# Performance work log

Hardware: AMD Instinct MI355X
Metric: run time of the kernel (lower is better)

The kernel has to match this reference:

```python
import jax, jax.numpy as jnp
import numpy as np

H, KV, D, HID = 32, 8, 128, 4096
B, S = 1, 2048
ROPE_THETA = 10000.0


def setup_inputs() -> dict:
    key = jax.random.key(0)
    ks = jax.random.split(key, 5)
    std = 0.02
    return {
        "x": jax.random.normal(ks[0], (B, S, HID), jnp.float32),
        "Wq": jax.random.normal(ks[1], (H * D, HID), jnp.float32) * std,
        "Wk": jax.random.normal(ks[2], (KV * D, HID), jnp.float32) * std,
        "Wv": jax.random.normal(ks[3], (KV * D, HID), jnp.float32) * std,
        "Wo": jax.random.normal(ks[4], (HID, H * D), jnp.float32) * std,
    }


def _rope_cos_sin(seq_len, dim, dtype):
    inv_freq = 1.0 / (ROPE_THETA ** (jnp.arange(0, dim, 2, dtype=jnp.float32) / dim))
    t = jnp.arange(seq_len, dtype=jnp.float32)
    freqs = jnp.einsum("s,d->sd", t, inv_freq)          # [S, D/2]
    emb = jnp.concatenate([freqs, freqs], axis=-1)        # [S, D]
    return jnp.cos(emb).astype(dtype), jnp.sin(emb).astype(dtype)


def _rotate_half(x):
    x1, x2 = jnp.split(x, 2, axis=-1)
    return jnp.concatenate([-x2, x1], axis=-1)


def reference(x, Wq, Wk, Wv, Wo):
    Bx, Sx, _ = x.shape
    q = (x @ Wq.T).reshape(Bx, Sx, H, D).transpose(0, 2, 1, 3)    # [B,H,S,D]
    k = (x @ Wk.T).reshape(Bx, Sx, KV, D).transpose(0, 2, 1, 3)   # [B,KV,S,D]
    v = (x @ Wv.T).reshape(Bx, Sx, KV, D).transpose(0, 2, 1, 3)

    cos, sin = _rope_cos_sin(Sx, D, x.dtype)                       # [S,D]
    q = q * cos + _rotate_half(q) * sin
    k = k * cos + _rotate_half(k) * sin

    rep = H // KV
    k = jnp.repeat(k, rep, axis=1)                                 # [B,H,S,D]
    v = jnp.repeat(v, rep, axis=1)

    scale = 1.0 / jnp.sqrt(jnp.asarray(D, x.dtype))
    scores = jnp.einsum("bhqd,bhkd->bhqk", q, k) * scale           # [B,H,S,S]
    causal = jnp.tril(jnp.ones((Sx, Sx), dtype=bool))
    scores = jnp.where(causal, scores, jnp.asarray(-1e30, x.dtype))
    attn = jax.nn.softmax(scores, axis=-1)
    out = jnp.einsum("bhqk,bhkd->bhqd", attn, v)                   # [B,H,S,D]
    out = out.transpose(0, 2, 1, 3).reshape(Bx, Sx, H * D)
    return out @ Wo.T
```

## Files before the change

kernel.cpp:

```cpp
#include <hip/hip_runtime.h>

typedef unsigned short u16;
typedef unsigned int u32;

using f32x4  = __attribute__((ext_vector_type(4))) float;
using f32x16 = __attribute__((ext_vector_type(16))) float;
using bf16x8 = __attribute__((ext_vector_type(8))) __bf16;

#define S_LEN 2048
#define HID_DIM 4096
#define NH 32
#define NKV 8
#define HD 128
#define QKVN 6144

__device__ __forceinline__ u16 f2b(float f) {
  union { float f; u32 u; } v; v.f = f;
  u32 r = (v.u + 0x7FFFu + ((v.u >> 16) & 1u)) >> 16;
  return (u16)r;
}
__device__ __forceinline__ float b2f(u16 b) {
  union { u32 u; float f; } v; v.u = ((u32)b) << 16;
  return v.f;
}

__device__ __forceinline__ u32 cvtpk_bf16(float lo, float hi) {
  u32 r;
  asm("v_cvt_pk_bf16_f32 %0, %1, %2" : "=v"(r) : "v"(lo), "v"(hi));
  return r;
}
__device__ __forceinline__ void plane_swap(u32& a, u32& b) {
  asm volatile("v_permlane32_swap_b32 %0, %1" : "+v"(a), "+v"(b));
}

#define AS1 __attribute__((address_space(1)))
#define AS3 __attribute__((address_space(3)))
__device__ __forceinline__ void gl_lds16(const u16* g, u16* l) {
  __builtin_amdgcn_global_load_lds((const AS1 u32*)g, (AS3 u32*)l, 16, 0, 0);
}

#define SBAR  __builtin_amdgcn_s_barrier()
#define SCHED0 __builtin_amdgcn_sched_barrier(0)
#define LGKM0 do { asm volatile("s_waitcnt lgkmcnt(0)" ::: "memory"); SCHED0; } while (0)
#define PRIO1 __builtin_amdgcn_s_setprio(1)
#define PRIO0 __builtin_amdgcn_s_setprio(0)

template <int N> __device__ __forceinline__ void waitv() {
  if constexpr (N == 0) asm volatile("s_waitcnt vmcnt(0)" ::: "memory");
  else if constexpr (N == 6) asm volatile("s_waitcnt vmcnt(6)" ::: "memory");
  else if constexpr (N == 7) asm volatile("s_waitcnt vmcnt(7)" ::: "memory");
  else asm volatile("s_waitcnt vmcnt(0)" ::: "memory");
  SCHED0;
}

__global__ void cast_kernel(const float* __restrict__ src, u16* __restrict__ dst, int n4) {
  int i = blockIdx.x * blockDim.x + threadIdx.x;
  int stride = gridDim.x * blockDim.x;
  for (; i < n4; i += stride) {
    float4 v = ((const float4*)src)[i];
    uint2 o;
    o.x = (u32)f2b(v.x) | ((u32)f2b(v.y) << 16);
    o.y = (u32)f2b(v.z) | ((u32)f2b(v.w) << 16);
    ((uint2*)dst)[i] = o;
  }
}

#define STAGE(DST, SRC, CH, LDK)                                   \
  _Pragma("unroll") for (int c = 0; c < (CH); ++c) {               \
    int d_ = c * 8192 + tid * 16;                                  \
    int rw_ = d_ >> 7;                                             \
    int cb_ = (d_ & 127) ^ ((rw_ & 7) << 4);                       \
    gl_lds16((SRC) + (size_t)rw_ * (LDK) + (cb_ >> 1), (DST) + (d_ >> 1)); \
  }

#define READ_A(ABUF, MLO)                                                     \
  _Pragma("unroll") for (int mm = 0; mm < 4; ++mm)                            \
  _Pragma("unroll") for (int ks = 0; ks < 2; ++ks)                            \
    af[(MLO) + mm][ks] = *(const bf16x8*)((const char*)(ABUF) +               \
      (wmo + ((MLO) + mm) * 16 + lr) * 128 + ((((ks << 2) | lg) ^ lr7) << 4));

#define READ_B(BBUF, KS)                                                      \
  _Pragma("unroll") for (int nn = 0; nn < NF; ++nn)                           \
    bfr[nn][KS] = *(const bf16x8*)((const char*)(BBUF) +                      \
      (wno + nn * 16 + lr) * 128 + (((((KS) << 2) | lg) ^ lr7) << 4));

#define MFMA_Q(MLO, KS)                                                       \
  _Pragma("unroll") for (int mm = 0; mm < 4; ++mm)                            \
  _Pragma("unroll") for (int nn = 0; nn < NF; ++nn)                           \
    acc[(MLO) + mm][nn] = __builtin_amdgcn_mfma_f32_16x16x32_bf16(            \
        af[(MLO) + mm][KS], bfr[nn][KS], acc[(MLO) + mm][nn], 0, 0, 0);

template <int BN, int WN, int CBF>
__global__ __launch_bounds__(512, 2) void gemm8p(
    const u16* __restrict__ A, const u16* __restrict__ B, void* __restrict__ Cout,
    int M, int N, int K)
{
  constexpr int BM = 256;
  constexpr int NF = WN / 16;
  constexpr int LA = BM / 64;
  constexpr int LB = BN / 64;
  constexpr int LT = LA + LB;
  extern __shared__ __align__(16) u16 smem[];
  u16* const As0 = smem;
  u16* const Bs0 = smem + 2 * BM * 64;

  const int tid  = threadIdx.x;
  const int lane = tid & 63;
  const int wave = tid >> 6;
  const int lr  = lane & 15;
  const int lg  = lane >> 4;
  const int lr7 = lane & 7;

  const int nbx = N / BN;
  const int bid = blockIdx.x;
  const int cpx = gridDim.x >> 3;
  const int swz = (bid & 7) * cpx + (bid >> 3);
  const int bm = (swz / nbx) * BM;
  const int bn = (swz % nbx) * BN;
  const int wmo = (wave >> 2) * 128;
  const int wno = (wave & 3) * WN;

  const int NT = K >> 6;

  f32x4 acc[8][NF] = {};
  bf16x8 af[8][2], bfr[NF][2];

  const u16* aP = A + (size_t)bm * K;
  const u16* bP = B + (size_t)bn * K;

  STAGE(As0,               aP,      LA, K);
  STAGE(Bs0,               bP,      LB, K);
  STAGE(As0 + BM * 64,     aP + 64, LA, K);
  STAGE(Bs0 + BN * 64,     bP + 64, LB, K);
  waitv<LT>();
  SBAR; SCHED0;

  for (int t = 0; t < NT; ++t) {
    const int buf = t & 1;
    const u16* ab = As0 + buf * (BM * 64);
    const u16* bb = Bs0 + buf * (BN * 64);
    const bool st = (t + 2 < NT);

    READ_A(ab, 0);
    READ_B(bb, 0);
    SCHED0; SBAR; LGKM0;
    PRIO1; MFMA_Q(0, 0); PRIO0;
    SBAR; SCHED0;

    READ_A(ab, 4);
    READ_B(bb, 1);
    SCHED0; SBAR; LGKM0;
    PRIO1; MFMA_Q(4, 0); PRIO0;
    SBAR; SCHED0;

    if (st) {
      const u16* aS = aP + (size_t)(t + 2) * 64;
      u16* aD = As0 + buf * (BM * 64);
      STAGE(aD, aS, LA, K);
    }
    SCHED0; SBAR;
    PRIO1; MFMA_Q(0, 1); PRIO0;
    SBAR; SCHED0;

    if (st) {
      const u16* bS = bP + (size_t)(t + 2) * 64;
      u16* bD = Bs0 + buf * (BN * 64);
      STAGE(bD, bS, LB, K);
    }
    SCHED0; SBAR;
    PRIO1; MFMA_Q(4, 1); PRIO0;
    if (t + 1 < NT) {
      if (t < NT - 3) waitv<LT>(); else waitv<0>();
    }
    SBAR; SCHED0;
  }

#pragma unroll
  for (int m = 0; m < 8; ++m)
#pragma unroll
    for (int j = 0; j < 4; ++j) {
      int row = bm + wmo + m * 16 + lg * 4 + j;
      size_t base = (size_t)row * N + bn + wno + lr;
      if constexpr (CBF) {
        u16* C = (u16*)Cout;
#pragma unroll
        for (int nn = 0; nn < NF; ++nn) C[base + nn * 16] = f2b(acc[m][nn][j]);
      } else {
        float* C = (float*)Cout;
#pragma unroll
        for (int nn = 0; nn < NF; ++nn) C[base + nn * 16] = acc[m][nn][j];
      }
    }
}

__global__ void rope_qk(const u16* __restrict__ qkv, u16* __restrict__ dst,
                        int col_off, float scale, int frag) {
  int idx = blockIdx.x * blockDim.x + threadIdx.x;
  int i = idx & 63;
  int s = (idx >> 6) & (S_LEN - 1);
  int h = idx >> 17;
  const u16* row = qkv + (size_t)s * QKVN + col_off + h * HD;
  float a = b2f(row[i]);
  float b = b2f(row[i + 64]);
  float invf = __expf(-(float)i * 0.14391156831212787f);
  float f = (float)s * invf;
  float sn, cs;
  sincosf(f, &sn, &cs);
  float o1 = (a * cs - b * sn) * scale;
  float o2 = (b * cs + a * sn) * scale;
  if (frag) {
    int qt = h * 64 + (s >> 5);
    int qq = s & 31;
    int i2 = i + 64;
    dst[((qt * 8 + (i  >> 4)) * 2 + ((i  >> 3) & 1)) * 256 + qq * 8 + (i  & 7)] = f2b(o1);
    dst[((qt * 8 + (i2 >> 4)) * 2 + ((i2 >> 3) & 1)) * 256 + qq * 8 + (i2 & 7)] = f2b(o2);
  } else {
    u16* orow = dst + ((size_t)h * S_LEN + s) * HD;
    orow[i]      = f2b(o1);
    orow[i + 64] = f2b(o2);
  }
}

__global__ __launch_bounds__(256) void vf_pack(const u16* __restrict__ qkv,
                                               u16* __restrict__ VF) {
  __shared__ u16 vlds[32][136];
  const int bid = blockIdx.x;
  const int kv = bid >> 6, t = bid & 63;
  const int tid = threadIdx.x;
  const int r = tid >> 3, d0 = (tid & 7) * 16;
  const u16* src = qkv + (size_t)(t * 32 + r) * QKVN + 5120 + kv * HD + d0;
  *(bf16x8*)&vlds[r][d0]     = *(const bf16x8*)src;
  *(bf16x8*)&vlds[r][d0 + 8] = *(const bf16x8*)(src + 8);
  __syncthreads();
  u16* outt = VF + (size_t)bid * 4096;
#pragma unroll
  for (int g = 0; g < 2; ++g) {
    int G = tid + g * 256;
    int q = G & 31, dt = (G >> 5) & 3, hi2 = (G >> 7) & 1, kc = G >> 8;
    union { u16 u[8]; uint4 v; } o;
#pragma unroll
    for (int e = 0; e < 8; ++e)
      o.u[e] = vlds[kc * 16 + hi2 * 8 + e][dt * 32 + q];
    *(uint4*)&outt[G * 8] = o.v;
  }
}

__global__ __launch_bounds__(256, 2) void attn_fwd(
    const u16* __restrict__ QF,
    const u16* __restrict__ KF,
    const u16* __restrict__ VF,
    u16* __restrict__ Out)
{
  const int tid  = threadIdx.x;
  const int lane = tid & 63;
  const int wv   = tid >> 6;
  const int q31  = lane & 31;
  const int hi   = lane >> 5;
  const int bid  = blockIdx.x;
  const int kvh  = bid & 7;
  const int qi   = 63 - (bid >> 3);
  const int q0   = qi * 32;
  const int h    = kvh * 4 + wv;
  const int nt   = qi + 1;

  const u16* kbase = KF + (size_t)kvh * 64 * 4096 + hi * 256  + q31 * 8;
  const u16* vbase = VF + (size_t)kvh * 64 * 4096 + hi * 1024 + q31 * 8;

  bf16x8 qf[8];
  const u16* qfp = QF + (size_t)(h * 64 + qi) * 4096 + hi * 256 + q31 * 8;
#pragma unroll
  for (int dc = 0; dc < 8; ++dc)
    qf[dc] = *(const bf16x8*)(qfp + dc * 512);

  f32x16 o0 = {}, o1 = {}, o2 = {}, o3 = {};
  float m = -1e30f, lsum = 0.f;

  for (int t = 0; t < nt; ++t) {
    SBAR;

    bf16x8 kf[8];
    const u16* kfp = kbase + (size_t)t * 4096;
#pragma unroll
    for (int dc = 0; dc < 8; ++dc)
      kf[dc] = *(const bf16x8*)(kfp + dc * 512);

    bf16x8 vf[8];
    const u16* vfp = vbase + (size_t)t * 4096;
#pragma unroll
    for (int i = 0; i < 8; ++i)
      vf[i] = *(const bf16x8*)(vfp + (i & 1) * 2048 + (i >> 1) * 256);

    f32x16 st = {};
    PRIO1;
#pragma unroll
    for (int dc = 0; dc < 8; ++dc)
      st = __builtin_amdgcn_mfma_f32_32x32x16_bf16(kf[dc], qf[dc], st, 0, 0, 0);
    PRIO0;

    if (t == nt - 1) {
#pragma unroll
      for (int r = 0; r < 16; ++r) {
        int kk = (r & 3) + 8 * (r >> 2) + 4 * hi;
        if (kk > q31) st[r] = -1e30f;
      }
    }

    float a0 = fmaxf(st[0], st[1]),   a1 = fmaxf(st[2], st[3]);
    float a2 = fmaxf(st[4], st[5]),   a3 = fmaxf(st[6], st[7]);
    float a4 = fmaxf(st[8], st[9]),   a5 = fmaxf(st[10], st[11]);
    float a6 = fmaxf(st[12], st[13]), a7 = fmaxf(st[14], st[15]);
    a0 = fmaxf(a0, a1); a2 = fmaxf(a2, a3); a4 = fmaxf(a4, a5); a6 = fmaxf(a6, a7);
    float pmax = fmaxf(fmaxf(a0, a2), fmaxf(a4, a6));
    pmax = fmaxf(pmax, __shfl_xor(pmax, 32));

    if (__any(pmax > m + 8.f)) {
      float mn = fmaxf(m, pmax);
      float sf = exp2f(m - mn);
      m = mn;
      lsum *= sf;
#pragma unroll
      for (int r = 0; r < 16; ++r) { o0[r] *= sf; o1[r] *= sf; o2[r] *= sf; o3[r] *= sf; }
    }

    float ev[16];
#pragma unroll
    for (int r = 0; r < 16; ++r) ev[r] = exp2f(st[r] - m);
    float s0 = (ev[0] + ev[1]) + (ev[2] + ev[3]);
    float s1 = (ev[4] + ev[5]) + (ev[6] + ev[7]);
    float s2 = (ev[8] + ev[9]) + (ev[10] + ev[11]);
    float s3 = (ev[12] + ev[13]) + (ev[14] + ev[15]);
    float ps = (s0 + s1) + (s2 + s3);
    ps += __shfl_xor(ps, 32);
    lsum += ps;

    u32 c0 = cvtpk_bf16(ev[0],  ev[1]),  c1 = cvtpk_bf16(ev[2],  ev[3]);
    u32 c2 = cvtpk_bf16(ev[4],  ev[5]),  c3 = cvtpk_bf16(ev[6],  ev[7]);
    u32 c4 = cvtpk_bf16(ev[8],  ev[9]),  c5 = cvtpk_bf16(ev[10], ev[11]);
    u32 c6 = cvtpk_bf16(ev[12], ev[13]), c7 = cvtpk_bf16(ev[14], ev[15]);
    plane_swap(c0, c2);
    plane_swap(c1, c3);
    plane_swap(c4, c6);
    plane_swap(c5, c7);
    union { u32 u[4]; bf16x8 v; } pb0u, pb1u;
    pb0u.u[0] = c0; pb0u.u[1] = c1; pb0u.u[2] = c2; pb0u.u[3] = c3;
    pb1u.u[0] = c4; pb1u.u[1] = c5; pb1u.u[2] = c6; pb1u.u[3] = c7;

    PRIO1;
    o0 = __builtin_amdgcn_mfma_f32_32x32x16_bf16(vf[0], pb0u.v, o0, 0, 0, 0);
    o1 = __builtin_amdgcn_mfma_f32_32x32x16_bf16(vf[2], pb0u.v, o1, 0, 0, 0);
    o2 = __builtin_amdgcn_mfma_f32_32x32x16_bf16(vf[4], pb0u.v, o2, 0, 0, 0);
    o3 = __builtin_amdgcn_mfma_f32_32x32x16_bf16(vf[6], pb0u.v, o3, 0, 0, 0);
    o0 = __builtin_amdgcn_mfma_f32_32x32x16_bf16(vf[1], pb1u.v, o0, 0, 0, 0);
    o1 = __builtin_amdgcn_mfma_f32_32x32x16_bf16(vf[3], pb1u.v, o1, 0, 0, 0);
    o2 = __builtin_amdgcn_mfma_f32_32x32x16_bf16(vf[5], pb1u.v, o2, 0, 0, 0);
    o3 = __builtin_amdgcn_mfma_f32_32x32x16_bf16(vf[7], pb1u.v, o3, 0, 0, 0);
    PRIO0;
  }

  float inv = 1.0f / lsum;
  u16* orow = Out + (size_t)(q0 + q31) * (NH * HD) + h * HD;
#pragma unroll
  for (int dt = 0; dt < 4; ++dt) {
    const f32x16& oo = dt == 0 ? o0 : dt == 1 ? o1 : dt == 2 ? o2 : o3;
#pragma unroll
    for (int g = 0; g < 4; ++g) {
      ushort4 pk;
      pk.x = f2b(oo[g * 4 + 0] * inv);
      pk.y = f2b(oo[g * 4 + 1] * inv);
      pk.z = f2b(oo[g * 4 + 2] * inv);
      pk.w = f2b(oo[g * 4 + 3] * inv);
      *(ushort4*)&orow[dt * 32 + 8 * g + 4 * hi] = pk;
    }
  }
}

extern "C" void kernel_launch(void* const* d_in, const int* in_sizes, int n_in,
                              void* d_out, int out_size, void* d_ws, size_t ws_size,
                              hipStream_t stream) {
  const float* x  = (const float*)d_in[0];
  const float* Wq = (const float*)d_in[1];
  const float* Wk = (const float*)d_in[2];
  const float* Wv = (const float*)d_in[3];
  const float* Wo = (const float*)d_in[4];
  float* out = (float*)d_out;

  char* ws = (char*)d_ws;
  u16* xb   = (u16*)(ws);
  u16* wqkv = (u16*)(ws + (16ull << 20));
  u16* wo_b = (u16*)(ws + (64ull << 20));
  u16* qkvb = (u16*)(ws + (96ull << 20));
  u16* qb   = (u16*)(ws + (16ull << 20));
  u16* kfb  = (u16*)(ws + (32ull << 20));
  u16* vfb  = (u16*)(ws + (36ull << 20));
  u16* ao   = (u16*)(ws);

  const int smem_q = (256 + 192) * 256;
  const int smem_o = (256 + 128) * 256;
  hipFuncSetAttribute((const void*)&gemm8p<192, 48, 1>,
                      hipFuncAttributeMaxDynamicSharedMemorySize, smem_q);
  hipFuncSetAttribute((const void*)&gemm8p<128, 32, 0>,
                      hipFuncAttributeMaxDynamicSharedMemorySize, smem_o);

  cast_kernel<<<4096, 256, 0, stream>>>(x,  xb,   (2048 * 4096) / 4);
  cast_kernel<<<4096, 256, 0, stream>>>(Wq, wqkv, (4096 * 4096) / 4);
  cast_kernel<<<2048, 256, 0, stream>>>(Wk, wqkv + (size_t)4096 * 4096, (1024 * 4096) / 4);
  cast_kernel<<<2048, 256, 0, stream>>>(Wv, wqkv + (size_t)5120 * 4096, (1024 * 4096) / 4);
  cast_kernel<<<4096, 256, 0, stream>>>(Wo, wo_b, (4096 * 4096) / 4);

  gemm8p<192, 48, 1><<<256, 512, smem_q, stream>>>(xb, wqkv, qkvb, 2048, 6144, 4096);

  rope_qk<<<(32 * 2048 * 64) / 256, 256, 0, stream>>>(qkvb, qb,  0,    0.12751741f, 1);
  rope_qk<<<(8  * 2048 * 64) / 256, 256, 0, stream>>>(qkvb, kfb, 4096, 1.0f,        1);
  vf_pack<<<512, 256, 0, stream>>>(qkvb, vfb);

  attn_fwd<<<512, 256, 0, stream>>>(qb, kfb, vfb, ao);

  gemm8p<128, 32, 0><<<256, 512, smem_o, stream>>>(ao, wo_b, out, 2048, 4096, 4096);
}
```

Baseline: 328.1 us.

## Replace 8-wave 256-row GEMM with 4-wave 128-row tile GEMM

Both projection GEMMs switch from a 512-thread, 256-row block tile to a 256-thread, 128-row block tile with 2x2 waves, which doubles the grid to 512 blocks. The inner loop is simplified: two K-substeps, each reading A and B fragments and issuing all MFMAs, followed by staging the next K tile and waiting. The aim is better CU occupancy and load balance with more blocks and fewer registers per thread. The cost is lower operand reuse per block, more global and LDS traffic per FLOP, and less interleaving of global loads with MFMA work.

```diff
diff --git a/kernel.cpp b/kernel.cpp
--- a/kernel.cpp
+++ b/kernel.cpp
@@ -46,10 +46,12 @@
 #define PRIO0 __builtin_amdgcn_s_setprio(0)
 
 template <int N> __device__ __forceinline__ void waitv() {
-  if constexpr (N == 0) asm volatile("s_waitcnt vmcnt(0)" ::: "memory");
-  else if constexpr (N == 6) asm volatile("s_waitcnt vmcnt(6)" ::: "memory");
-  else if constexpr (N == 7) asm volatile("s_waitcnt vmcnt(7)" ::: "memory");
-  else asm volatile("s_waitcnt vmcnt(0)" ::: "memory");
+  if constexpr (N == 0)       asm volatile("s_waitcnt vmcnt(0)"  ::: "memory");
+  else if constexpr (N == 6)  asm volatile("s_waitcnt vmcnt(6)"  ::: "memory");
+  else if constexpr (N == 7)  asm volatile("s_waitcnt vmcnt(7)"  ::: "memory");
+  else if constexpr (N == 8)  asm volatile("s_waitcnt vmcnt(8)"  ::: "memory");
+  else if constexpr (N == 10) asm volatile("s_waitcnt vmcnt(10)" ::: "memory");
+  else                        asm volatile("s_waitcnt vmcnt(0)"  ::: "memory");
   SCHED0;
 }
 
@@ -65,44 +67,47 @@
   }
 }
 
-#define STAGE(DST, SRC, CH, LDK)                                   \
+
+#define STG(DST, SRC, CH, LDK)                                     \
   _Pragma("unroll") for (int c = 0; c < (CH); ++c) {               \
-    int d_ = c * 8192 + tid * 16;                                  \
+    int d_ = c * 4096 + tid * 16;                                  \
     int rw_ = d_ >> 7;                                             \
     int cb_ = (d_ & 127) ^ ((rw_ & 7) << 4);                       \
     gl_lds16((SRC) + (size_t)rw_ * (LDK) + (cb_ >> 1), (DST) + (d_ >> 1)); \
   }
 
-#define READ_A(ABUF, MLO)                                                     \
+#define RD_A(ABUF, KS)                                                        \
   _Pragma("unroll") for (int mm = 0; mm < 4; ++mm)                            \
-  _Pragma("unroll") for (int ks = 0; ks < 2; ++ks)                            \
-    af[(MLO) + mm][ks] = *(const bf16x8*)((const char*)(ABUF) +               \
-      (wmo + ((MLO) + mm) * 16 + lr) * 128 + ((((ks << 2) | lg) ^ lr7) << 4));
-
-#define READ_B(BBUF, KS)                                                      \
+    af[mm] = *(const bf16x8*)((const char*)(ABUF) +                           \
+      (wmo + mm * 16 + lr) * 128 + ((((KS) * 4 + lg) ^ lr7) << 4));
+
+#define RD_B(BBUF, KS)                                                        \
   _Pragma("unroll") for (int nn = 0; nn < NF; ++nn)                           \
-    bfr[nn][KS] = *(const bf16x8*)((const char*)(BBUF) +                      \
-      (wno + nn * 16 + lr) * 128 + (((((KS) << 2) | lg) ^ lr7) << 4));
-
-#define MFMA_Q(MLO, KS)                                                       \
+    bfr[nn] = *(const bf16x8*)((const char*)(BBUF) +                          \
+      (wno + nn * 16 + lr) * 128 + ((((KS) * 4 + lg) ^ lr7) << 4));
+
+#define MFMA_ALL                                                              \
   _Pragma("unroll") for (int mm = 0; mm < 4; ++mm)                            \
   _Pragma("unroll") for (int nn = 0; nn < NF; ++nn)                           \
-    acc[(MLO) + mm][nn] = __builtin_amdgcn_mfma_f32_16x16x32_bf16(            \
-        af[(MLO) + mm][KS], bfr[nn][KS], acc[(MLO) + mm][nn], 0, 0, 0);
-
-template <int BN, int WN, int CBF>
-__global__ __launch_bounds__(512, 2) void gemm8p(
+    acc[mm][nn] = __builtin_amdgcn_mfma_f32_16x16x32_bf16(                    \
+        af[mm], bfr[nn], acc[mm][nn], 0, 0, 0);
+
+template <int BN, int CBF>
+__global__ __launch_bounds__(256, 2) void gemm2b(
     const u16* __restrict__ A, const u16* __restrict__ B, void* __restrict__ Cout,
     int M, int N, int K)
 {
-  constexpr int BM = 256;
+  constexpr int BM = 128;
+  constexpr int WN = BN / 2;
   constexpr int NF = WN / 16;
-  constexpr int LA = BM / 64;
-  constexpr int LB = BN / 64;
+  constexpr int LA = (BM * 128) / 4096;
+  constexpr int LB = (BN * 128) / 4096;
   constexpr int LT = LA + LB;
+  constexpr int ASZ = BM * 64;
+  constexpr int BSZ = BN * 64;
   extern __shared__ __align__(16) u16 smem[];
   u16* const As0 = smem;
-  u16* const Bs0 = smem + 2 * BM * 64;
+  u16* const Bs0 = smem + 2 * ASZ;
 
   const int tid  = threadIdx.x;
   const int lane = tid & 63;
@@ -117,78 +122,64 @@
   const int swz = (bid & 7) * cpx + (bid >> 3);
   const int bm = (swz / nbx) * BM;
   const int bn = (swz % nbx) * BN;
-  const int wmo = (wave >> 2) * 128;
-  const int wno = (wave & 3) * WN;
+  const int wmo = (wave >> 1) * 64;
+  const int wno = (wave & 1) * WN;
 
   const int NT = K >> 6;
 
-  f32x4 acc[8][NF] = {};
-  bf16x8 af[8][2], bfr[NF][2];
+  f32x4 acc[4][NF] = {};
+  bf16x8 af[4], bfr[NF];
 
   const u16* aP = A + (size_t)bm * K;
   const u16* bP = B + (size_t)bn * K;
 
-  STAGE(As0,               aP,      LA, K);
-  STAGE(Bs0,               bP,      LB, K);
-  STAGE(As0 + BM * 64,     aP + 64, LA, K);
-  STAGE(Bs0 + BN * 64,     bP + 64, LB, K);
+  STG(As0,        aP,      LA, K);
+  STG(Bs0,        bP,      LB, K);
+  STG(As0 + ASZ,  aP + 64, LA, K);
+  STG(Bs0 + BSZ,  bP + 64, LB, K);
   waitv<LT>();
   SBAR; SCHED0;
 
   for (int t = 0; t < NT; ++t) {
     const int buf = t & 1;
-    const u16* ab = As0 + buf * (BM * 64);
-    const u16* bb = Bs0 + buf * (BN * 64);
+    const u16* ab = As0 + buf * ASZ;
+    const u16* bb = Bs0 + buf * BSZ;
+
+    RD_A(ab, 0); RD_B(bb, 0);
+    SCHED0; SBAR; LGKM0;
+    PRIO1; MFMA_ALL; PRIO0;
+    SBAR; SCHED0;
+
+    RD_A(ab, 1); RD_B(bb, 1);
+    SCHED0; SBAR; LGKM0;
+    PRIO1; MFMA_ALL; PRIO0;
+    SBAR; SCHED0;
+
     const bool st = (t + 2 < NT);
-
-    READ_A(ab, 0);
-    READ_B(bb, 0);
-    SCHED0; SBAR; LGKM0;
-    PRIO1; MFMA_Q(0, 0); PRIO0;
+    if (st) {
+      STG(As0 + buf * ASZ, aP + (size_t)(t + 2) * 64, LA, K);
+      STG(Bs0 + buf * BSZ, bP + (size_t)(t + 2) * 64, LB, K);
+    }
+    if (t + 1 < NT) {
+      if (st) waitv<LT>(); else waitv<0>();
+    }
     SBAR; SCHED0;
-
-    READ_A(ab, 4);
-    READ_B(bb, 1);
-    SCHED0; SBAR; LGKM0;
-    PRIO1; MFMA_Q(4, 0); PRIO0;
-    SBAR; SCHED0;
-
-    if (st) {
-      const u16* aS = aP + (size_t)(t + 2) * 64;
-      u16* aD = As0 + buf * (BM * 64);
-      STAGE(aD, aS, LA, K);
-    }
-    SCHED0; SBAR;
-    PRIO1; MFMA_Q(0, 1); PRIO0;
-    SBAR; SCHED0;
-
-    if (st) {
-      const u16* bS = bP + (size_t)(t + 2) * 64;
-      u16* bD = Bs0 + buf * (BN * 64);
-      STAGE(bD, bS, LB, K);
-    }
-    SCHED0; SBAR;
-    PRIO1; MFMA_Q(4, 1); PRIO0;
-    if (t + 1 < NT) {
-      if (t < NT - 3) waitv<LT>(); else waitv<0>();
-    }
-    SBAR; SCHED0;
-  }
-
-#pragma unroll
-  for (int m = 0; m < 8; ++m)
+  }
+
+#pragma unroll
+  for (int mm = 0; mm < 4; ++mm)
 #pragma unroll
     for (int j = 0; j < 4; ++j) {
-      int row = bm + wmo + m * 16 + lg * 4 + j;
+      int row = bm + wmo + mm * 16 + lg * 4 + j;
       size_t base = (size_t)row * N + bn + wno + lr;
       if constexpr (CBF) {
         u16* C = (u16*)Cout;
 #pragma unroll
-        for (int nn = 0; nn < NF; ++nn) C[base + nn * 16] = f2b(acc[m][nn][j]);
+        for (int nn = 0; nn < NF; ++nn) C[base + nn * 16] = f2b(acc[mm][nn][j]);
       } else {
         float* C = (float*)Cout;
 #pragma unroll
-        for (int nn = 0; nn < NF; ++nn) C[base + nn * 16] = acc[m][nn][j];
+        for (int nn = 0; nn < NF; ++nn) C[base + nn * 16] = acc[mm][nn][j];
       }
     }
 }
@@ -394,11 +385,11 @@
   u16* vfb  = (u16*)(ws + (36ull << 20));
   u16* ao   = (u16*)(ws);
 
-  const int smem_q = (256 + 192) * 256;
-  const int smem_o = (256 + 128) * 256;
-  hipFuncSetAttribute((const void*)&gemm8p<192, 48, 1>,
+  const int smem_q = (128 + 192) * 64 * 2 * 2;
+  const int smem_o = (128 + 128) * 64 * 2 * 2;
+  hipFuncSetAttribute((const void*)&gemm2b<192, 1>,
                       hipFuncAttributeMaxDynamicSharedMemorySize, smem_q);
-  hipFuncSetAttribute((const void*)&gemm8p<128, 32, 0>,
+  hipFuncSetAttribute((const void*)&gemm2b<128, 0>,
                       hipFuncAttributeMaxDynamicSharedMemorySize, smem_o);
 
   cast_kernel<<<4096, 256, 0, stream>>>(x,  xb,   (2048 * 4096) / 4);
@@ -407,7 +398,7 @@
   cast_kernel<<<2048, 256, 0, stream>>>(Wv, wqkv + (size_t)5120 * 4096, (1024 * 4096) / 4);
   cast_kernel<<<4096, 256, 0, stream>>>(Wo, wo_b, (4096 * 4096) / 4);
 
-  gemm8p<192, 48, 1><<<256, 512, smem_q, stream>>>(xb, wqkv, qkvb, 2048, 6144, 4096);
+  gemm2b<192, 1><<<512, 256, smem_q, stream>>>(xb, wqkv, qkvb, 2048, 6144, 4096);
 
   rope_qk<<<(32 * 2048 * 64) / 256, 256, 0, stream>>>(qkvb, qb,  0,    0.12751741f, 1);
   rope_qk<<<(8  * 2048 * 64) / 256, 256, 0, stream>>>(qkvb, kfb, 4096, 1.0f,        1);
@@ -415,5 +406,5 @@
 
   attn_fwd<<<512, 256, 0, stream>>>(qb, kfb, vfb, ao);
 
-  gemm8p<128, 32, 0><<<256, 512, smem_o, stream>>>(ao, wo_b, out, 2048, 4096, 4096);
-}
+  gemm2b<128, 0><<<512, 256, smem_o, stream>>>(ao, wo_b, out, 2048, 4096, 4096);
+}
```

Measured after the change: 343.5 us. +4.7%, slower.

## Restructure GEMM main loop to cut barriers and batch LDS reads per k-slice

Applied to the files above, without the earlier changes.

Reorders the double-buffered GEMM inner loop so all A and B fragments for one k-slice are read from LDS at once, followed by all MFMAs for that slice. Both next-tile global-to-LDS stages are issued together after a single barrier, replacing the earlier four-phase schedule that had a barrier around every MFMA group. The aim is less barrier stall time and less interleaving overhead, at the cost of coarser overlap between LDS reads, global loads and MFMA. It also keeps more fragment registers live at once.

```diff
diff --git a/kernel.cpp b/kernel.cpp
--- a/kernel.cpp
+++ b/kernel.cpp
@@ -46,10 +46,10 @@
 #define PRIO0 __builtin_amdgcn_s_setprio(0)
 
 template <int N> __device__ __forceinline__ void waitv() {
-  if constexpr (N == 0) asm volatile("s_waitcnt vmcnt(0)" ::: "memory");
+  if constexpr (N == 0)      asm volatile("s_waitcnt vmcnt(0)" ::: "memory");
   else if constexpr (N == 6) asm volatile("s_waitcnt vmcnt(6)" ::: "memory");
   else if constexpr (N == 7) asm volatile("s_waitcnt vmcnt(7)" ::: "memory");
-  else asm volatile("s_waitcnt vmcnt(0)" ::: "memory");
+  else                       asm volatile("s_waitcnt vmcnt(0)" ::: "memory");
   SCHED0;
 }
 
@@ -65,6 +65,7 @@
   }
 }
 
+
 #define STAGE(DST, SRC, CH, LDK)                                   \
   _Pragma("unroll") for (int c = 0; c < (CH); ++c) {               \
     int d_ = c * 8192 + tid * 16;                                  \
@@ -73,13 +74,12 @@
     gl_lds16((SRC) + (size_t)rw_ * (LDK) + (cb_ >> 1), (DST) + (d_ >> 1)); \
   }
 
-#define READ_A(ABUF, MLO)                                                     \
+#define RDA(ABUF, MLO, KS)                                                    \
   _Pragma("unroll") for (int mm = 0; mm < 4; ++mm)                            \
-  _Pragma("unroll") for (int ks = 0; ks < 2; ++ks)                            \
-    af[(MLO) + mm][ks] = *(const bf16x8*)((const char*)(ABUF) +               \
-      (wmo + ((MLO) + mm) * 16 + lr) * 128 + ((((ks << 2) | lg) ^ lr7) << 4));
-
-#define READ_B(BBUF, KS)                                                      \
+    af[(MLO) + mm][KS] = *(const bf16x8*)((const char*)(ABUF) +               \
+      (wmo + ((MLO) + mm) * 16 + lr) * 128 + (((((KS) << 2) | lg) ^ lr7) << 4));
+
+#define RDB(BBUF, KS)                                                         \
   _Pragma("unroll") for (int nn = 0; nn < NF; ++nn)                           \
     bfr[nn][KS] = *(const bf16x8*)((const char*)(BBUF) +                      \
       (wno + nn * 16 + lr) * 128 + (((((KS) << 2) | lg) ^ lr7) << 4));
@@ -128,10 +128,10 @@
   const u16* aP = A + (size_t)bm * K;
   const u16* bP = B + (size_t)bn * K;
 
-  STAGE(As0,               aP,      LA, K);
-  STAGE(Bs0,               bP,      LB, K);
-  STAGE(As0 + BM * 64,     aP + 64, LA, K);
-  STAGE(Bs0 + BN * 64,     bP + 64, LB, K);
+  STAGE(As0,           aP,      LA, K);
+  STAGE(Bs0,           bP,      LB, K);
+  STAGE(As0 + BM * 64, aP + 64, LA, K);
+  STAGE(Bs0 + BN * 64, bP + 64, LB, K);
   waitv<LT>();
   SBAR; SCHED0;
 
@@ -141,36 +141,20 @@
     const u16* bb = Bs0 + buf * (BN * 64);
     const bool st = (t + 2 < NT);
 
-    READ_A(ab, 0);
-    READ_B(bb, 0);
-    SCHED0; SBAR; LGKM0;
-    PRIO1; MFMA_Q(0, 0); PRIO0;
-    SBAR; SCHED0;
-
-    READ_A(ab, 4);
-    READ_B(bb, 1);
-    SCHED0; SBAR; LGKM0;
-    PRIO1; MFMA_Q(4, 0); PRIO0;
-    SBAR; SCHED0;
+    RDA(ab, 0, 0); RDA(ab, 4, 0); RDB(bb, 0);
+    LGKM0;
+    PRIO1; MFMA_Q(0, 0); MFMA_Q(4, 0); PRIO0;
+    RDA(ab, 0, 1); RDA(ab, 4, 1); RDB(bb, 1);
+    LGKM0;
+    SBAR;
 
     if (st) {
-      const u16* aS = aP + (size_t)(t + 2) * 64;
-      u16* aD = As0 + buf * (BM * 64);
-      STAGE(aD, aS, LA, K);
-    }
-    SCHED0; SBAR;
-    PRIO1; MFMA_Q(0, 1); PRIO0;
-    SBAR; SCHED0;
-
-    if (st) {
-      const u16* bS = bP + (size_t)(t + 2) * 64;
-      u16* bD = Bs0 + buf * (BN * 64);
-      STAGE(bD, bS, LB, K);
-    }
-    SCHED0; SBAR;
-    PRIO1; MFMA_Q(4, 1); PRIO0;
+      STAGE(As0 + buf * (BM * 64), aP + (size_t)(t + 2) * 64, LA, K);
+      STAGE(Bs0 + buf * (BN * 64), bP + (size_t)(t + 2) * 64, LB, K);
+    }
+    PRIO1; MFMA_Q(0, 1); MFMA_Q(4, 1); PRIO0;
     if (t + 1 < NT) {
-      if (t < NT - 3) waitv<LT>(); else waitv<0>();
+      if (st) waitv<LT>(); else waitv<0>();
     }
     SBAR; SCHED0;
   }
```

New measurement: 312.9 us. 1.05x faster.
